# Kernel optimization log

Measured on AMD Instinct MI355X. Metric: run time of the kernel, lower is better.

The kernel has to match this reference:

```python
import jax, jax.numpy as jnp
import numpy as np

N = 10000      # nodes (drugs)
F_IN = 128     # input feature dim
H1 = 64        # hidden1
H2 = 32        # hidden2
R = 65         # num_relations
E_O = 320000   # edges in main graph
E_S = 160000   # edges per augmented subgraph
NB = 4         # num_layers parallel branches
B = 4096       # drug pairs


def setup_inputs() -> dict:
    key = jax.random.key(0)
    ks = jax.random.split(key, 32)
    def nrm(k, shape, fan_in):
        return (jax.random.normal(k, shape) * (1.0 / np.sqrt(fan_in))).astype(jnp.float32)
    inp = {}
    inp["x_o"] = jax.random.normal(ks[0], (N, F_IN), jnp.float32)
    inp["edge_index_o"] = jax.random.randint(ks[1], (2, E_O), 0, N)
    inp["edge_type_o"] = jax.random.randint(ks[2], (E_O,), 0, R)
    inp["x_s"] = jax.random.normal(ks[3], (NB, N, F_IN), jnp.float32)
    inp["edge_index_s"] = jax.random.randint(ks[4], (NB, 2, E_S), 0, N)
    inp["edge_type_s"] = jax.random.randint(ks[5], (NB, E_S), 0, R)
    inp["idx"] = jax.random.randint(ks[6], (2, B), 0, N)
    inp["features1"] = jax.random.normal(ks[7], (N, F_IN), jnp.float32)
    # main encoder RGCN params
    inp["W1"] = nrm(ks[8], (R, F_IN, H1), F_IN)
    inp["root1"] = nrm(ks[9], (F_IN, H1), F_IN)
    inp["b1"] = jnp.zeros((H1,), jnp.float32)
    inp["W2"] = nrm(ks[10], (R, H1, H2), H1)
    inp["root2"] = nrm(ks[11], (H1, H2), H1)
    inp["b2"] = jnp.zeros((H2,), jnp.float32)
    # 4 branch encoders (stacked over branch dim)
    inp["Ws1"] = nrm(ks[12], (NB, R, F_IN, H1), F_IN)
    inp["roots1"] = nrm(ks[13], (NB, F_IN, H1), F_IN)
    inp["bs1"] = jnp.zeros((NB, H1), jnp.float32)
    inp["Ws2"] = nrm(ks[14], (NB, R, H1, H2), H1)
    inp["roots2"] = nrm(ks[15], (NB, H1, H2), H1)
    inp["bs2"] = jnp.zeros((NB, H2), jnp.float32)
    # MLP head: 576 -> 256 -> 128 -> 65
    inp["mlp_w1"] = nrm(ks[16], (576, 256), 576)
    inp["mlp_b1"] = jnp.zeros((256,), jnp.float32)
    inp["mlp_w2"] = nrm(ks[17], (256, 128), 256)
    inp["mlp_b2"] = jnp.zeros((128,), jnp.float32)
    inp["mlp_w3"] = nrm(ks[18], (128, 65), 128)
    inp["mlp_b3"] = jnp.zeros((65,), jnp.float32)
    return inp


def _rgcn(x, src, dst, etype, W, Wroot, b):
    """PyG RGCNConv with aggr='mean': per-(dst,relation) mean of W_r x_j, summed over relations, plus root transform."""
    n = x.shape[0]
    r = W.shape[0]
    h = jnp.einsum('ni,rio->nro', x, W)                      # [N,R,out]
    seg = dst * r + etype                                    # per-(node,rel) segment id
    ones = jnp.ones(src.shape[0], x.dtype)
    deg = jax.ops.segment_sum(ones, seg, num_segments=n * r)  # in-degree per (dst,rel)
    norm = 1.0 / jnp.maximum(deg, 1.0)
    m = h[src, etype] * norm[seg][:, None]                   # [E,out]
    agg = jax.ops.segment_sum(m, dst, num_segments=n)        # scatter-add to dst
    return agg + x @ Wroot + b


def _branch(xb, src, dst, et, W1b, r1b, b1b, W2b, r2b, b2b):
    h1 = jax.nn.relu(_rgcn(xb, src, dst, et, W1b, r1b, b1b))
    return _rgcn(h1, src, dst, et, W2b, r2b, b2b)


def reference(x_o, edge_index_o, edge_type_o, x_s, edge_index_s, edge_type_s, idx,
              features1, W1, root1, b1, W2, root2, b2,
              Ws1, roots1, bs1, Ws2, roots2, bs2,
              mlp_w1, mlp_b1, mlp_w2, mlp_b2, mlp_w3, mlp_b3):
    # main encoder (dropout is eval-mode identity)
    src_o, dst_o = edge_index_o[0], edge_index_o[1]
    h1 = jax.nn.relu(_rgcn(x_o, src_o, dst_o, edge_type_o, W1, root1, b1))
    x2_oo = _rgcn(h1, src_o, dst_o, edge_type_o, W2, root2, b2)   # [N,H2]
    # 4 parallel branch encoders, vmapped over branch dim
    x2_s = jax.vmap(_branch)(x_s, edge_index_s[:, 0], edge_index_s[:, 1], edge_type_s,
                             Ws1, roots1, bs1, Ws2, roots2, bs2)  # [NB,N,H2]
    n = x2_oo.shape[0]
    embeds = jnp.concatenate(
        [x2_oo, jnp.transpose(x2_s, (1, 0, 2)).reshape(n, -1)], axis=1)  # [N, 5*H2]
    d1, d2 = idx[0], idx[1]
    feats = jnp.concatenate(
        [embeds[d1], features1[d1], embeds[d2], features1[d2]], axis=1)  # [B,576]
    h = jax.nn.elu(feats @ mlp_w1 + mlp_b1)
    h = jax.nn.elu(h @ mlp_w2 + mlp_b2)
    return h @ mlp_w3 + mlp_b3  # [B,65] logits
```

## Files before the change

kernel.cpp:

```cpp
#include <hip/hip_runtime.h>
#include <hip/hip_bf16.h>

namespace {
constexpr int N_NODES = 10000;
constexpr int FIN  = 128;
constexpr int H1S  = 64;
constexpr int H2S  = 32;
constexpr int RREL = 65;
constexpr int EO   = 320000;
constexpr int ES   = 160000;
constexpr int NBR  = 4;
constexpr int BP   = 4096;
constexpr int E_TOT = EO + 4 * ES;
constexpr int CAP_MAIN = EO + 128 * RREL;
constexpr int CAP_SUB  = ES + 128 * RREL;
constexpr int CAP_TOT  = CAP_MAIN + 4 * CAP_SUB;
constexpr int CHK_MAIN = CAP_MAIN / 128;
constexpr int CHK_SUB  = CAP_SUB / 128;
constexpr int CHK_TOT  = CHK_MAIN + 4 * CHK_SUB;
constexpr int CHK_TOT_PAD = 7840;
constexpr int SCH = 1024;
constexpr int SBLK_MAIN = (EO + SCH - 1) / SCH;
}

typedef unsigned short u16;
typedef unsigned int   u32;
typedef unsigned long long u64;
typedef short bf16x8 __attribute__((ext_vector_type(8)));
typedef float f32x4  __attribute__((ext_vector_type(4)));

__device__ __forceinline__ u16 f2bf(float f) {
    u32 u = __builtin_bit_cast(u32, f);
    u32 r = u + 0x7FFFu + ((u >> 16) & 1u);
    return (u16)(r >> 16);
}
__device__ __forceinline__ float bf2f_lo(u32 v) { return __builtin_bit_cast(float, v << 16); }
__device__ __forceinline__ float bf2f_hi(u32 v) { return __builtin_bit_cast(float, v & 0xFFFF0000u); }
__device__ __forceinline__ bf16x8 as_bf16x8(uint4 v) {
    union { uint4 u; bf16x8 b; } cv; cv.u = v; return cv.b;
}
__device__ __forceinline__ int chunk_graph(int bid) {
    return (bid < CHK_MAIN) ? 0 : 1 + (bid - CHK_MAIN) / CHK_SUB;
}

__global__ __launch_bounds__(256) void count_hist_all(const int* __restrict__ et_o,
                                                      const int* __restrict__ et_s,
                                                      int* __restrict__ hist) {
    int g = blockIdx.y;
    const int* etv; int E;
    if (g == 0) { etv = et_o; E = EO; }
    else { etv = et_s + (size_t)(g - 1) * ES; E = ES; }
    __shared__ int lh[RREL];
    for (int i = threadIdx.x; i < RREL; i += 256) lh[i] = 0;
    __syncthreads();
    for (int e = blockIdx.x * 256 + threadIdx.x; e < E; e += gridDim.x * 256)
        atomicAdd(&lh[etv[e]], 1);
    __syncthreads();
    for (int i = threadIdx.x; i < RREL; i += 256) {
        int c = lh[i];
        if (c) atomicAdd(&hist[g * RREL + i], c);
    }
}

__global__ void prefix_fill(const int* __restrict__ hist, int* __restrict__ cursor,
                            int* __restrict__ relbase, int* __restrict__ c2r) {
    int g = blockIdx.x;
    __shared__ int offs[RREL + 1];
    int capc  = (g == 0) ? CHK_MAIN : CHK_SUB;
    int cbase = (g == 0) ? 0 : CHK_MAIN + (g - 1) * CHK_SUB;
    int ebase = (g == 0) ? 0 : CAP_MAIN + (g - 1) * CAP_SUB;
    if (threadIdx.x == 0) {
        int acc = 0;
        for (int r = 0; r < RREL; ++r) {
            offs[r] = acc;
            cursor[g * RREL + r]  = ebase + acc;
            relbase[g * RREL + r] = ebase + acc;
            int c = hist[g * RREL + r];
            acc += (c + 127) & ~127;
        }
        offs[RREL] = acc;
    }
    __syncthreads();
    int total = offs[RREL];
    for (int c = threadIdx.x; c < capc; c += blockDim.x) {
        int pos = c * 128;
        int r = -1;
        if (pos < total) {
            int lo = 0, hi = RREL - 1;
            while (lo < hi) { int mid = (lo + hi + 1) >> 1; if (offs[mid] <= pos) lo = mid; else hi = mid - 1; }
            r = lo;
        }
        c2r[cbase + c] = r;
    }
}

__global__ __launch_bounds__(256) void scatter_rel(const int* __restrict__ ei_o,
                                                   const int* __restrict__ et_o,
                                                   const int* __restrict__ ei_s,
                                                   const int* __restrict__ et_s,
                                                   int* __restrict__ cursor,
                                                   int* __restrict__ ssrc,
                                                   int* __restrict__ sdst) {
    int g = blockIdx.y;
    const int* srcv; const int* dstv; const int* etv; int E;
    if (g == 0) { srcv = ei_o; dstv = ei_o + EO; etv = et_o; E = EO; }
    else {
        int b = g - 1;
        srcv = ei_s + (size_t)b * 2 * ES;
        dstv = srcv + ES;
        etv  = et_s + (size_t)b * ES;
        E = ES;
    }
    __shared__ int lh[RREL];
    __shared__ int lbase[RREL];
    int tid = threadIdx.x;
    int e0 = blockIdx.x * SCH;
    if (e0 >= E) return;
    int e1 = min(e0 + SCH, E);
    for (int i = tid; i < RREL; i += 256) lh[i] = 0;
    __syncthreads();
    for (int e = e0 + tid; e < e1; e += 256)
        atomicAdd(&lh[etv[e]], 1);
    __syncthreads();
    for (int i = tid; i < RREL; i += 256) {
        int c = lh[i];
        lbase[i] = c ? atomicAdd(&cursor[g * RREL + i], c) : 0;
        lh[i] = 0;
    }
    __syncthreads();
    for (int e = e0 + tid; e < e1; e += 256) {
        int r = etv[e];
        int rank = atomicAdd(&lh[r], 1);
        int pos = lbase[r] + rank;
        ssrc[pos] = srcv[e];
        sdst[pos] = dstv[e];
    }
}

__global__ __launch_bounds__(256) void seg_hist(const int* __restrict__ sdst,
                                                const int* __restrict__ relbase,
                                                const int* __restrict__ hist,
                                                u32* __restrict__ deg_r) {
    int r = blockIdx.x, g = blockIdx.y;
    __shared__ u32 h[N_NODES];
    int tid = threadIdx.x;
    for (int i = tid; i < N_NODES; i += 256) h[i] = 0;
    __syncthreads();
    int start = relbase[g * RREL + r], cnt = hist[g * RREL + r];
    for (int i = start + tid; i < start + cnt; i += 256)
        atomicAdd(&h[sdst[i]], 1u);
    __syncthreads();
    u32* out = deg_r + (size_t)(g * RREL + r) * N_NODES;
    for (int i = tid; i < N_NODES; i += 256) out[i] = h[i];
}

__global__ __launch_bounds__(256) void nodedeg_from_degr(const u32* __restrict__ deg_r,
                                                         int* __restrict__ node_deg) {
    int t = blockIdx.x * 256 + threadIdx.x;
    if (t >= 5 * N_NODES) return;
    int g = t / N_NODES, d = t % N_NODES;
    const u32* base = deg_r + (size_t)g * RREL * N_NODES + d;
    u32 s = 0;
    for (int r = 0; r < RREL; ++r) s += base[(size_t)r * N_NODES];
    node_deg[t] = (int)s;
}

__global__ __launch_bounds__(256) void scan_rowptr(const int* __restrict__ node_deg,
                                                   int* __restrict__ row_ptr) {
    int g = blockIdx.x;
    const int* nd = node_deg + (size_t)g * N_NODES;
    int* rp = row_ptr + (size_t)g * (N_NODES + 1);
    int off = (g == 0) ? 0 : EO + (g - 1) * ES;
    __shared__ int part[257];
    int tid = threadIdx.x;
    const int CH = (N_NODES + 255) / 256;
    int base = tid * CH;
    int s = 0;
    for (int i = 0; i < CH; ++i) { int ix = base + i; if (ix < N_NODES) s += nd[ix]; }
    part[tid + 1] = s;
    if (tid == 0) part[0] = 0;
    __syncthreads();
    if (tid == 0) { for (int i = 1; i <= 256; ++i) part[i] += part[i - 1]; }
    __syncthreads();
    int acc = part[tid];
    for (int i = 0; i < CH; ++i) {
        int ix = base + i;
        if (ix < N_NODES) { rp[ix] = off + acc; acc += nd[ix]; }
    }
    if (tid == 0) rp[N_NODES] = off + part[256];
}

__global__ __launch_bounds__(256) void drbase(const u32* __restrict__ deg_r,
                                              const int* __restrict__ row_ptr,
                                              u32* __restrict__ base_abs) {
    int t = blockIdx.x * 256 + threadIdx.x;
    if (t >= 5 * N_NODES) return;
    int g = t / N_NODES, d = t % N_NODES;
    u32 run = (u32)row_ptr[(size_t)g * (N_NODES + 1) + d];
    const u32* din = deg_r + (size_t)g * RREL * N_NODES + d;
    u32* bout = base_abs + (size_t)g * RREL * N_NODES + d;
    for (int r = 0; r < RREL; ++r) {
        bout[(size_t)r * N_NODES] = run;
        run += din[(size_t)r * N_NODES];
    }
}

__global__ __launch_bounds__(256) void snrm_epos(const int* __restrict__ sdst,
                                                 const int* __restrict__ relbase,
                                                 const int* __restrict__ hist,
                                                 const u32* __restrict__ base_abs,
                                                 const u32* __restrict__ deg_r,
                                                 int* __restrict__ epos,
                                                 float* __restrict__ snrm) {
    int r = blockIdx.x, g = blockIdx.y;
    int cnt = hist[g * RREL + r];
    if (cnt == 0) return;
    __shared__ u32 cur[N_NODES];
    __shared__ u16 dg[N_NODES];
    int tid = threadIdx.x;
    const u32* bslice = base_abs + (size_t)(g * RREL + r) * N_NODES;
    const u32* dslice = deg_r + (size_t)(g * RREL + r) * N_NODES;
    for (int i = tid; i < N_NODES; i += 256) {
        cur[i] = bslice[i];
        dg[i] = (u16)dslice[i];
    }
    __syncthreads();
    int start = relbase[g * RREL + r];
    for (int pos = start + tid; pos < start + cnt; pos += 256) {
        int d = sdst[pos];
        u32 slot = atomicAdd(&cur[d], 1u);
        epos[pos] = (int)slot;
        snrm[pos] = 1.0f / fmaxf((float)dg[d], 1.0f);
    }
}

namespace {
constexpr int NX_  = 5 * N_NODES * FIN;
constexpr int NW1_ = 5 * RREL * FIN * H1S;
constexpr int NW2_ = 5 * RREL * H1S * H2S;
constexpr int NM1_ = 256 * 576;
constexpr int NM2_ = 128 * 256;
constexpr int NM3_ = 128 * 128;
constexpr int NPREP = NX_ + NW1_ + NW2_ + NM1_ + NM2_ + NM3_;
}
__global__ __launch_bounds__(256) void prep_all(const float* __restrict__ x_o,
                                                const float* __restrict__ x_s,
                                                const float* __restrict__ W1,
                                                const float* __restrict__ Ws1,
                                                const float* __restrict__ W2,
                                                const float* __restrict__ Ws2,
                                                const float* __restrict__ mw1,
                                                const float* __restrict__ mw2,
                                                const float* __restrict__ mw3,
                                                u16* __restrict__ xbf,
                                                u16* __restrict__ wt1,
                                                u16* __restrict__ wt2,
                                                u16* __restrict__ w1t,
                                                u16* __restrict__ w2t,
                                                u16* __restrict__ w3t) {
    int t = blockIdx.x * 256 + threadIdx.x;
    if (t < NX_) {
        int g = t / (N_NODES * FIN), off = t % (N_NODES * FIN);
        float v = (g == 0) ? x_o[off] : x_s[(size_t)(g - 1) * N_NODES * FIN + off];
        xbf[t] = f2bf(v);
        return;
    }
    t -= NX_;
    if (t < NW1_) {
        int q = t % (RREL * FIN * H1S), g = t / (RREL * FIN * H1S);
        int k = q & 127; int ro = q >> 7; int o = ro & 63; int r = ro >> 6;
        const float* src = (g == 0) ? W1 : Ws1 + (size_t)(g - 1) * RREL * FIN * H1S;
        wt1[(size_t)g * RREL * FIN * H1S + q] = f2bf(src[((size_t)r * FIN + k) * H1S + o]);
        return;
    }
    t -= NW1_;
    if (t < NW2_) {
        int q = t % (RREL * H1S * H2S), g = t / (RREL * H1S * H2S);
        int k = q & 63; int ro = q >> 6; int o = ro & 31; int r = ro >> 5;
        const float* src = (g == 0) ? W2 : Ws2 + (size_t)(g - 1) * RREL * H1S * H2S;
        wt2[(size_t)g * RREL * H1S * H2S + q] = f2bf(src[((size_t)r * H1S + k) * H2S + o]);
        return;
    }
    t -= NW2_;
    if (t < NM1_) {
        int k = t % 576, o = t / 576;
        w1t[t] = f2bf(mw1[(size_t)k * 256 + o]);
        return;
    }
    t -= NM1_;
    if (t < NM2_) {
        int k = t % 256, o = t / 256;
        w2t[t] = f2bf(mw2[(size_t)k * 128 + o]);
        return;
    }
    t -= NM2_;
    if (t < NM3_) {
        int k = t % 128, o = t / 128;
        w3t[t] = (o < 65) ? f2bf(mw3[(size_t)k * 65 + o]) : (u16)0;
    }
}

__global__ __launch_bounds__(256) void rgcn_mfma_l1_all(const u16* __restrict__ xbfa,
                                                        const int* __restrict__ ssrc,
                                                        const float* __restrict__ snrm,
                                                        const int* __restrict__ c2r,
                                                        const int* __restrict__ epos,
                                                        const u16* __restrict__ wt1a,
                                                        u16* __restrict__ medge) {
    __shared__ uint4 Wt4[64 * 16];
    int tid = threadIdx.x;
    int bid = blockIdx.x;
    int r = c2r[bid];
    if (r < 0) return;
    int g = chunk_graph(bid);
    int e0 = bid * 128;
    const u16* xbf = xbfa + (size_t)g * N_NODES * FIN;
    {
        const uint4* wsrc = (const uint4*)(wt1a + ((size_t)g * RREL + r) * H1S * FIN);
        #pragma unroll
        for (int i = 0; i < 4; ++i) {
            int g16 = tid + i * 256;
            int row = g16 >> 4, c = g16 & 15;
            Wt4[row * 16 + (c ^ (row & 7))] = wsrc[g16];
        }
    }
    int w = tid >> 6, l = tid & 63;
    int lo = l & 15, hi = l >> 4;
    int ea = w * 32 + lo, eb = ea + 16;
    int sa = ssrc[e0 + ea], sb = ssrc[e0 + eb];
    const uint4* xa = (const uint4*)(xbf + (size_t)sa * FIN);
    const uint4* xb = (const uint4*)(xbf + (size_t)sb * FIN);
    __syncthreads();
    f32x4 acc[2][4];
    #pragma unroll
    for (int m = 0; m < 2; ++m)
        #pragma unroll
        for (int n = 0; n < 4; ++n) acc[m][n] = {0.f, 0.f, 0.f, 0.f};
    #pragma unroll
    for (int kk = 0; kk < 4; ++kk) {
        int kc = kk * 4 + hi;
        bf16x8 a0 = as_bf16x8(xa[kc]);
        bf16x8 a1 = as_bf16x8(xb[kc]);
        #pragma unroll
        for (int n = 0; n < 4; ++n) {
            int o = n * 16 + lo;
            bf16x8 b = as_bf16x8(Wt4[o * 16 + (kc ^ (o & 7))]);
            acc[0][n] = __builtin_amdgcn_mfma_f32_16x16x32_bf16(a0, b, acc[0][n], 0, 0, 0);
            acc[1][n] = __builtin_amdgcn_mfma_f32_16x16x32_bf16(a1, b, acc[1][n], 0, 0, 0);
        }
    }
    #pragma unroll
    for (int m = 0; m < 2; ++m) {
        #pragma unroll
        for (int rg = 0; rg < 4; ++rg) {
            int erow = e0 + w * 32 + m * 16 + hi * 4 + rg;
            float nv = snrm[erow];
            if (nv != 0.f) {
                size_t jb = (size_t)epos[erow] * H1S;
                #pragma unroll
                for (int n = 0; n < 4; ++n)
                    __builtin_nontemporal_store(f2bf(acc[m][n][rg] * nv),
                                                medge + jb + n * 16 + lo);
            }
        }
    }
}

__global__ __launch_bounds__(256) void rgcn_mfma_l2_all(const u16* __restrict__ h1bfa,
                                                        const int* __restrict__ ssrc,
                                                        const float* __restrict__ snrm,
                                                        const int* __restrict__ c2r,
                                                        const int* __restrict__ epos,
                                                        const u16* __restrict__ wt2a,
                                                        u16* __restrict__ medge) {
    __shared__ uint4 Wt4[32 * 8];
    int tid = threadIdx.x;
    int bid = blockIdx.x;
    int r = c2r[bid];
    if (r < 0) return;
    int g = chunk_graph(bid);
    int e0 = bid * 128;
    const u16* h1bf = h1bfa + (size_t)g * N_NODES * H1S;
    {
        const uint4* wsrc = (const uint4*)(wt2a + ((size_t)g * RREL + r) * H2S * H1S);
        int row = tid >> 3, c = tid & 7;
        Wt4[row * 8 + (c ^ (row & 7))] = wsrc[tid];
    }
    int w = tid >> 6, l = tid & 63;
    int lo = l & 15, hi = l >> 4;
    int ea = w * 32 + lo, eb = ea + 16;
    int sa = ssrc[e0 + ea], sb = ssrc[e0 + eb];
    const uint4* xa = (const uint4*)(h1bf + (size_t)sa * H1S);
    const uint4* xb = (const uint4*)(h1bf + (size_t)sb * H1S);
    __syncthreads();
    f32x4 acc[2][2];
    #pragma unroll
    for (int m = 0; m < 2; ++m)
        #pragma unroll
        for (int n = 0; n < 2; ++n) acc[m][n] = {0.f, 0.f, 0.f, 0.f};
    #pragma unroll
    for (int kk = 0; kk < 2; ++kk) {
        int kc = kk * 4 + hi;
        bf16x8 a0 = as_bf16x8(xa[kc]);
        bf16x8 a1 = as_bf16x8(xb[kc]);
        #pragma unroll
        for (int n = 0; n < 2; ++n) {
            int o = n * 16 + lo;
            bf16x8 b = as_bf16x8(Wt4[o * 8 + (kc ^ (o & 7))]);
            acc[0][n] = __builtin_amdgcn_mfma_f32_16x16x32_bf16(a0, b, acc[0][n], 0, 0, 0);
            acc[1][n] = __builtin_amdgcn_mfma_f32_16x16x32_bf16(a1, b, acc[1][n], 0, 0, 0);
        }
    }
    #pragma unroll
    for (int m = 0; m < 2; ++m) {
        #pragma unroll
        for (int rg = 0; rg < 4; ++rg) {
            int erow = e0 + w * 32 + m * 16 + hi * 4 + rg;
            float nv = snrm[erow];
            if (nv != 0.f) {
                size_t jb = (size_t)epos[erow] * H2S;
                #pragma unroll
                for (int n = 0; n < 2; ++n)
                    __builtin_nontemporal_store(f2bf(acc[m][n][rg] * nv),
                                                medge + jb + n * 16 + lo);
            }
        }
    }
}

__global__ __launch_bounds__(256) void finish_l1_all(const float* __restrict__ x_o,
                                                     const float* __restrict__ x_s,
                                                     const float* __restrict__ root1,
                                                     const float* __restrict__ roots1,
                                                     const float* __restrict__ b1,
                                                     const float* __restrict__ bs1,
                                                     const u16* __restrict__ medge,
                                                     const int* __restrict__ row_ptr,
                                                     float* __restrict__ aggH1,
                                                     u16* __restrict__ h1bfa) {
    int g = blockIdx.y;
    const float* x    = (g == 0) ? x_o : x_s + (size_t)(g - 1) * N_NODES * FIN;
    const float* root = (g == 0) ? root1 : roots1 + (size_t)(g - 1) * FIN * H1S;
    const float* bias = (g == 0) ? b1 : bs1 + (size_t)(g - 1) * H1S;
    const int* rp = row_ptr + (size_t)g * (N_NODES + 1);
    float* h1 = aggH1 + (size_t)g * N_NODES * H1S;
    u16* h1bf = h1bfa + (size_t)g * N_NODES * H1S;
    __shared__ float xs[16][FIN + 1];
    int tid = threadIdx.x;
    int vsub = tid >> 4, og = tid & 15;
    int v = blockIdx.x * 16 + vsub;
    bool valid = v < N_NODES;
    int vv = valid ? v : N_NODES - 1;
    #pragma unroll
    for (int i = 0; i < 8; ++i)
        xs[vsub][og + 16 * i] = x[(size_t)vv * FIN + og + 16 * i];
    int j0 = rp[vv], j1 = rp[vv + 1];
    float4 acc;
    acc.x = bias[og * 4 + 0]; acc.y = bias[og * 4 + 1];
    acc.z = bias[og * 4 + 2]; acc.w = bias[og * 4 + 3];
    for (int j = j0; j < j1; ++j) {
        u64 m = __builtin_nontemporal_load(
            (const u64*)(medge + (size_t)j * H1S + og * 4));
        u32 mlo = (u32)m, mhi = (u32)(m >> 32);
        acc.x += bf2f_lo(mlo); acc.y += bf2f_hi(mlo);
        acc.z += bf2f_lo(mhi); acc.w += bf2f_hi(mhi);
    }
    __syncthreads();
    const float* Rp = root + og * 4;
    #pragma unroll 16
    for (int i = 0; i < FIN; ++i) {
        float xv = xs[vsub][i];
        float4 w = *(const float4*)(Rp + (size_t)i * H1S);
        acc.x += xv * w.x; acc.y += xv * w.y; acc.z += xv * w.z; acc.w += xv * w.w;
    }
    if (valid) {
        float r0 = fmaxf(acc.x, 0.f), r1 = fmaxf(acc.y, 0.f);
        float r2 = fmaxf(acc.z, 0.f), r3 = fmaxf(acc.w, 0.f);
        float* ag = h1 + (size_t)vv * H1S + og * 4;
        ag[0] = r0; ag[1] = r1; ag[2] = r2; ag[3] = r3;
        uint2 pk;
        pk.x = (u32)f2bf(r0) | ((u32)f2bf(r1) << 16);
        pk.y = (u32)f2bf(r2) | ((u32)f2bf(r3) << 16);
        *(uint2*)(h1bf + (size_t)vv * H1S + og * 4) = pk;
    }
}

__global__ __launch_bounds__(256) void finish_l2_all(const float* __restrict__ aggH1,
                                                     const float* __restrict__ root2,
                                                     const float* __restrict__ roots2,
                                                     const float* __restrict__ b2,
                                                     const float* __restrict__ bs2,
                                                     const u16* __restrict__ medge,
                                                     const int* __restrict__ row_ptr,
                                                     float* __restrict__ aggH2) {
    int g = blockIdx.y;
    const float* x    = aggH1 + (size_t)g * N_NODES * H1S;
    const float* root = (g == 0) ? root2 : roots2 + (size_t)(g - 1) * H1S * H2S;
    const float* bias = (g == 0) ? b2 : bs2 + (size_t)(g - 1) * H2S;
    const int* rp = row_ptr + (size_t)g * (N_NODES + 1);
    float* x2 = aggH2 + (size_t)g * N_NODES * H2S;
    __shared__ float xs[32][H1S + 1];
    int tid = threadIdx.x;
    int vsub = tid >> 3, og = tid & 7;
    int v = blockIdx.x * 32 + vsub;
    bool valid = v < N_NODES;
    int vv = valid ? v : N_NODES - 1;
    #pragma unroll
    for (int i = 0; i < 8; ++i)
        xs[vsub][og + 8 * i] = x[(size_t)vv * H1S + og + 8 * i];
    int j0 = rp[vv], j1 = rp[vv + 1];
    float4 acc;
    acc.x = bias[og * 4 + 0]; acc.y = bias[og * 4 + 1];
    acc.z = bias[og * 4 + 2]; acc.w = bias[og * 4 + 3];
    for (int j = j0; j < j1; ++j) {
        u64 m = __builtin_nontemporal_load(
            (const u64*)(medge + (size_t)j * H2S + og * 4));
        u32 mlo = (u32)m, mhi = (u32)(m >> 32);
        acc.x += bf2f_lo(mlo); acc.y += bf2f_hi(mlo);
        acc.z += bf2f_lo(mhi); acc.w += bf2f_hi(mhi);
    }
    __syncthreads();
    const float* Rp = root + og * 4;
    #pragma unroll
    for (int i = 0; i < H1S; ++i) {
        float xv = xs[vsub][i];
        float4 w = *(const float4*)(Rp + (size_t)i * H2S);
        acc.x += xv * w.x; acc.y += xv * w.y; acc.z += xv * w.z; acc.w += xv * w.w;
    }
    if (valid) {
        float* ag = x2 + (size_t)vv * H2S + og * 4;
        ag[0] = acc.x; ag[1] = acc.y; ag[2] = acc.z; ag[3] = acc.w;
    }
}

__global__ __launch_bounds__(256) void gather_feats_direct(const float* __restrict__ aggH2,
                                                           const float* __restrict__ features1,
                                                           const int* __restrict__ idx,
                                                           u16* __restrict__ featsbf) {
    int t = blockIdx.x * blockDim.x + threadIdx.x;
    if (t >= BP * 576) return;
    int b = t / 576, c = t % 576;
    int d1 = idx[b], d2 = idx[BP + b];
    float v;
    if (c < 160) {
        int bb = c >> 5, cc = c & 31;
        v = aggH2[(size_t)bb * N_NODES * H2S + (size_t)d1 * H2S + cc];
    } else if (c < 288) {
        v = features1[(size_t)d1 * FIN + (c - 160)];
    } else if (c < 448) {
        int cc2 = c - 288;
        int bb = cc2 >> 5, cc = cc2 & 31;
        v = aggH2[(size_t)bb * N_NODES * H2S + (size_t)d2 * H2S + cc];
    } else {
        v = features1[(size_t)d2 * FIN + (c - 448)];
    }
    featsbf[t] = f2bf(v);
}

template <int ACT, int OUTF>
__global__ __launch_bounds__(256) void mlp_mfma(const u16* __restrict__ A,
                                                const u16* __restrict__ Bt,
                                                const float* __restrict__ bias,
                                                u16* __restrict__ Cbf,
                                                float* __restrict__ Cf,
                                                int M, int N, int K) {
    __shared__ uint4 As4[128 * 8];
    __shared__ uint4 Bs4[64 * 8];
    int tid = threadIdx.x;
    int row0 = blockIdx.x * 128, col0 = blockIdx.y * 64;
    int w = tid >> 6, l = tid & 63;
    int lo = l & 15, hi = l >> 4;
    f32x4 acc[2][4];
    #pragma unroll
    for (int m = 0; m < 2; ++m)
        #pragma unroll
        for (int n = 0; n < 4; ++n) acc[m][n] = {0.f, 0.f, 0.f, 0.f};
    int nchunks = K >> 6;
    for (int ch = 0; ch < nchunks; ++ch) {
        #pragma unroll
        for (int i = 0; i < 4; ++i) {
            int g16 = tid + i * 256;
            int rr = g16 >> 3, c = g16 & 7;
            As4[rr * 8 + (c ^ (rr & 7))] =
                *((const uint4*)(A + (size_t)(row0 + rr) * K + ch * 64) + c);
        }
        #pragma unroll
        for (int i = 0; i < 2; ++i) {
            int g16 = tid + i * 256;
            int rr = g16 >> 3, c = g16 & 7;
            Bs4[rr * 8 + (c ^ (rr & 7))] =
                *((const uint4*)(Bt + (size_t)(col0 + rr) * K + ch * 64) + c);
        }
        __syncthreads();
        #pragma unroll
        for (int ks = 0; ks < 2; ++ks) {
            int kc = ks * 4 + hi;
            int ra = w * 32 + lo, rb = w * 32 + 16 + lo;
            bf16x8 a0 = as_bf16x8(As4[ra * 8 + (kc ^ (ra & 7))]);
            bf16x8 a1 = as_bf16x8(As4[rb * 8 + (kc ^ (rb & 7))]);
            #pragma unroll
            for (int n = 0; n < 4; ++n) {
                int o = n * 16 + lo;
                bf16x8 b = as_bf16x8(Bs4[o * 8 + (kc ^ (o & 7))]);
                acc[0][n] = __builtin_amdgcn_mfma_f32_16x16x32_bf16(a0, b, acc[0][n], 0, 0, 0);
                acc[1][n] = __builtin_amdgcn_mfma_f32_16x16x32_bf16(a1, b, acc[1][n], 0, 0, 0);
            }
        }
        __syncthreads();
    }
    #pragma unroll
    for (int m = 0; m < 2; ++m) {
        #pragma unroll
        for (int rg = 0; rg < 4; ++rg) {
            int rr = row0 + w * 32 + m * 16 + hi * 4 + rg;
            if (rr < M) {
                #pragma unroll
                for (int n = 0; n < 4; ++n) {
                    int cc = col0 + n * 16 + lo;
                    if (cc < N) {
                        float v = acc[m][n][rg] + bias[cc];
                        if (ACT == 1) v = (v > 0.f) ? v : expm1f(v);
                        if (OUTF) Cf[(size_t)rr * N + cc] = v;
                        else Cbf[(size_t)rr * N + cc] = f2bf(v);
                    }
                }
            }
        }
    }
}

extern "C" void kernel_launch(void* const* d_in, const int* in_sizes, int n_in,
                              void* d_out, int out_size, void* d_ws, size_t ws_size,
                              hipStream_t stream) {
    const float* x_o      = (const float*)d_in[0];
    const int*   ei_o     = (const int*)d_in[1];
    const int*   et_o     = (const int*)d_in[2];
    const float* x_s      = (const float*)d_in[3];
    const int*   ei_s     = (const int*)d_in[4];
    const int*   et_s     = (const int*)d_in[5];
    const int*   idx      = (const int*)d_in[6];
    const float* features1= (const float*)d_in[7];
    const float* W1       = (const float*)d_in[8];
    const float* root1    = (const float*)d_in[9];
    const float* b1       = (const float*)d_in[10];
    const float* W2       = (const float*)d_in[11];
    const float* root2    = (const float*)d_in[12];
    const float* b2       = (const float*)d_in[13];
    const float* Ws1      = (const float*)d_in[14];
    const float* roots1   = (const float*)d_in[15];
    const float* bs1      = (const float*)d_in[16];
    const float* Ws2      = (const float*)d_in[17];
    const float* roots2   = (const float*)d_in[18];
    const float* bs2      = (const float*)d_in[19];
    const float* mlp_w1   = (const float*)d_in[20];
    const float* mlp_b1   = (const float*)d_in[21];
    const float* mlp_w2   = (const float*)d_in[22];
    const float* mlp_b2   = (const float*)d_in[23];
    const float* mlp_w3   = (const float*)d_in[24];
    const float* mlp_b3   = (const float*)d_in[25];

    int*   hist     = (int*)d_ws;
    int*   ssrc     = hist + 5 * RREL;
    float* snrm     = (float*)(ssrc + CAP_TOT);
    int*   sdst     = (int*)(snrm + CAP_TOT);
    int*   cursor   = sdst + CAP_TOT;
    int*   relbase  = cursor + 5 * RREL;
    int*   c2r      = relbase + 5 * RREL;
    u32*   deg_r    = (u32*)(c2r + CHK_TOT_PAD);
    u32*   base_abs = deg_r + (size_t)5 * RREL * N_NODES;
    int*   node_deg = (int*)(base_abs + (size_t)5 * RREL * N_NODES);
    int*   row_ptr  = node_deg + 5 * N_NODES;
    int*   epos     = row_ptr + 5 * (N_NODES + 1);
    float* aggH1    = (float*)(epos + CAP_TOT);
    float* aggH2    = aggH1 + (size_t)5 * N_NODES * H1S;
    u16*   featsbf  = (u16*)(aggH2 + (size_t)5 * N_NODES * H2S);
    u16*   mh1bf    = featsbf + (size_t)BP * 576;
    u16*   mh2bf    = mh1bf + (size_t)BP * 256;
    u16*   w1t      = mh2bf + (size_t)BP * 128;
    u16*   w2t      = w1t + (size_t)256 * 576;
    u16*   w3t      = w2t + (size_t)128 * 256;
    u16*   wt1a     = w3t + (size_t)128 * 128;
    u16*   wt2a     = wt1a + (size_t)5 * RREL * H1S * FIN;
    u16*   xbfa     = wt2a + (size_t)5 * RREL * H2S * H1S;
    u16*   h1bfa    = xbfa + (size_t)5 * N_NODES * FIN;
    u16*   medge    = h1bfa + (size_t)5 * N_NODES * H1S;

    size_t zero_bytes = (size_t)((char*)sdst - (char*)d_ws);
    hipMemsetAsync(d_ws, 0, zero_bytes, stream);

    prep_all<<<(NPREP + 255) / 256, 256, 0, stream>>>(
        x_o, x_s, W1, Ws1, W2, Ws2, mlp_w1, mlp_w2, mlp_w3,
        xbfa, wt1a, wt2a, w1t, w2t, w3t);
    count_hist_all<<<dim3(128, 5), 256, 0, stream>>>(et_o, et_s, hist);
    prefix_fill<<<5, 256, 0, stream>>>(hist, cursor, relbase, c2r);
    scatter_rel<<<dim3(SBLK_MAIN, 5), 256, 0, stream>>>(
        ei_o, et_o, ei_s, et_s, cursor, ssrc, sdst);
    seg_hist<<<dim3(RREL, 5), 256, 0, stream>>>(sdst, relbase, hist, deg_r);
    nodedeg_from_degr<<<(5 * N_NODES + 255) / 256, 256, 0, stream>>>(deg_r, node_deg);
    scan_rowptr<<<5, 256, 0, stream>>>(node_deg, row_ptr);
    drbase<<<(5 * N_NODES + 255) / 256, 256, 0, stream>>>(deg_r, row_ptr, base_abs);
    snrm_epos<<<dim3(RREL, 5), 256, 0, stream>>>(
        sdst, relbase, hist, base_abs, deg_r, epos, snrm);

    rgcn_mfma_l1_all<<<CHK_TOT, 256, 0, stream>>>(
        xbfa, ssrc, snrm, c2r, epos, wt1a, medge);
    finish_l1_all<<<dim3((N_NODES + 15) / 16, 5), 256, 0, stream>>>(
        x_o, x_s, root1, roots1, b1, bs1, medge, row_ptr, aggH1, h1bfa);
    rgcn_mfma_l2_all<<<CHK_TOT, 256, 0, stream>>>(
        h1bfa, ssrc, snrm, c2r, epos, wt2a, medge);
    finish_l2_all<<<dim3((N_NODES + 31) / 32, 5), 256, 0, stream>>>(
        aggH1, root2, roots2, b2, bs2, medge, row_ptr, aggH2);

    gather_feats_direct<<<(BP * 576 + 255) / 256, 256, 0, stream>>>(aggH2, features1, idx, featsbf);
    mlp_mfma<1, 0><<<dim3(BP / 128, 4), 256, 0, stream>>>(featsbf, w1t, mlp_b1, mh1bf, nullptr, BP, 256, 576);
    mlp_mfma<1, 0><<<dim3(BP / 128, 2), 256, 0, stream>>>(mh1bf, w2t, mlp_b2, mh2bf, nullptr, BP, 128, 256);
    mlp_mfma<0, 1><<<dim3(BP / 128, 2), 256, 0, stream>>>(mh2bf, w3t, mlp_b3, nullptr, (float*)d_out, BP, 65, 128);
}
```

Measured before the change: 488.4 us.

## Stage gathered source rows in LDS and swizzle chunk blocks across XCDs

The layer-1 and layer-2 edge MFMA kernels now gather source-node feature rows cooperatively into swizzled shared memory. Two threads fetch each row with contiguous 64-byte reads, replacing the per-lane scattered 16-byte global loads that fed the MFMA fragments. Layer 1 stages its 128-wide rows in two halves to limit shared memory, which adds extra barriers. Block IDs are also remapped so that consecutive chunks, which share a relation weight and graph, land on the same XCD to improve L2 reuse of weights and features.

After: 519.0 us. +6.3%, slower.

```diff
diff --git a/kernel.cpp b/kernel.cpp
--- a/kernel.cpp
+++ b/kernel.cpp
@@ -41,6 +41,11 @@
 }
 __device__ __forceinline__ int chunk_graph(int bid) {
     return (bid < CHK_MAIN) ? 0 : 1 + (bid - CHK_MAIN) / CHK_SUB;
+}
+__device__ __forceinline__ int xcd_swz(int bid) {
+    constexpr int q = CHK_TOT / 8, rr = CHK_TOT % 8;
+    int x = bid & 7, i = bid >> 3;
+    return (x < rr ? x * (q + 1) : rr * (q + 1) + (x - rr) * q) + i;
 }
 
 __global__ __launch_bounds__(256) void count_hist_all(const int* __restrict__ et_o,
@@ -308,8 +313,9 @@
                                                         const u16* __restrict__ wt1a,
                                                         u16* __restrict__ medge) {
     __shared__ uint4 Wt4[64 * 16];
-    int tid = threadIdx.x;
-    int bid = blockIdx.x;
+    __shared__ uint4 Xs4[128 * 8];
+    int tid = threadIdx.x;
+    int bid = xcd_swz(blockIdx.x);
     int r = c2r[bid];
     if (r < 0) return;
     int g = chunk_graph(bid);
@@ -326,27 +332,37 @@
     }
     int w = tid >> 6, l = tid & 63;
     int lo = l & 15, hi = l >> 4;
-    int ea = w * 32 + lo, eb = ea + 16;
-    int sa = ssrc[e0 + ea], sb = ssrc[e0 + eb];
-    const uint4* xa = (const uint4*)(xbf + (size_t)sa * FIN);
-    const uint4* xb = (const uint4*)(xbf + (size_t)sb * FIN);
-    __syncthreads();
+    int rt = tid >> 1, ph = tid & 1;
+    int srow = ssrc[e0 + rt];
+    const uint4* xsrc = (const uint4*)(xbf + (size_t)srow * FIN);
     f32x4 acc[2][4];
     #pragma unroll
     for (int m = 0; m < 2; ++m)
         #pragma unroll
         for (int n = 0; n < 4; ++n) acc[m][n] = {0.f, 0.f, 0.f, 0.f};
     #pragma unroll
-    for (int kk = 0; kk < 4; ++kk) {
-        int kc = kk * 4 + hi;
-        bf16x8 a0 = as_bf16x8(xa[kc]);
-        bf16x8 a1 = as_bf16x8(xb[kc]);
-        #pragma unroll
-        for (int n = 0; n < 4; ++n) {
-            int o = n * 16 + lo;
-            bf16x8 b = as_bf16x8(Wt4[o * 16 + (kc ^ (o & 7))]);
-            acc[0][n] = __builtin_amdgcn_mfma_f32_16x16x32_bf16(a0, b, acc[0][n], 0, 0, 0);
-            acc[1][n] = __builtin_amdgcn_mfma_f32_16x16x32_bf16(a1, b, acc[1][n], 0, 0, 0);
+    for (int khalf = 0; khalf < 2; ++khalf) {
+        if (khalf) __syncthreads();
+        #pragma unroll
+        for (int j = 0; j < 4; ++j) {
+            int c = ph * 4 + j;
+            Xs4[rt * 8 + (c ^ (rt & 7))] = xsrc[khalf * 8 + c];
+        }
+        __syncthreads();
+        #pragma unroll
+        for (int kk2 = 0; kk2 < 2; ++kk2) {
+            int kc  = kk2 * 4 + hi;
+            int kcg = khalf * 8 + kc;
+            int ea = w * 32 + lo, eb = ea + 16;
+            bf16x8 a0 = as_bf16x8(Xs4[ea * 8 + (kc ^ (ea & 7))]);
+            bf16x8 a1 = as_bf16x8(Xs4[eb * 8 + (kc ^ (eb & 7))]);
+            #pragma unroll
+            for (int n = 0; n < 4; ++n) {
+                int o = n * 16 + lo;
+                bf16x8 b = as_bf16x8(Wt4[o * 16 + (kcg ^ (o & 7))]);
+                acc[0][n] = __builtin_amdgcn_mfma_f32_16x16x32_bf16(a0, b, acc[0][n], 0, 0, 0);
+                acc[1][n] = __builtin_amdgcn_mfma_f32_16x16x32_bf16(a1, b, acc[1][n], 0, 0, 0);
+            }
         }
     }
     #pragma unroll
@@ -373,9 +389,10 @@
                                                         const int* __restrict__ epos,
                                                         const u16* __restrict__ wt2a,
                                                         u16* __restrict__ medge) {
+    __shared__ uint4 Xs4[128 * 8];
     __shared__ uint4 Wt4[32 * 8];
     int tid = threadIdx.x;
-    int bid = blockIdx.x;
+    int bid = xcd_swz(blockIdx.x);
     int r = c2r[bid];
     if (r < 0) return;
     int g = chunk_graph(bid);
@@ -386,13 +403,19 @@
         int row = tid >> 3, c = tid & 7;
         Wt4[row * 8 + (c ^ (row & 7))] = wsrc[tid];
     }
+    {
+        int rt = tid >> 1, h = tid & 1;
+        int s = ssrc[e0 + rt];
+        const uint4* src = (const uint4*)(h1bf + (size_t)s * H1S) + h * 4;
+        #pragma unroll
+        for (int j = 0; j < 4; ++j) {
+            int c = h * 4 + j;
+            Xs4[rt * 8 + (c ^ (rt & 7))] = src[j];
+        }
+    }
+    __syncthreads();
     int w = tid >> 6, l = tid & 63;
     int lo = l & 15, hi = l >> 4;
-    int ea = w * 32 + lo, eb = ea + 16;
-    int sa = ssrc[e0 + ea], sb = ssrc[e0 + eb];
-    const uint4* xa = (const uint4*)(h1bf + (size_t)sa * H1S);
-    const uint4* xb = (const uint4*)(h1bf + (size_t)sb * H1S);
-    __syncthreads();
     f32x4 acc[2][2];
     #pragma unroll
     for (int m = 0; m < 2; ++m)
@@ -401,8 +424,9 @@
     #pragma unroll
     for (int kk = 0; kk < 2; ++kk) {
         int kc = kk * 4 + hi;
-        bf16x8 a0 = as_bf16x8(xa[kc]);
-        bf16x8 a1 = as_bf16x8(xb[kc]);
+        int ea = w * 32 + lo, eb = ea + 16;
+        bf16x8 a0 = as_bf16x8(Xs4[ea * 8 + (kc ^ (ea & 7))]);
+        bf16x8 a1 = as_bf16x8(Xs4[eb * 8 + (kc ^ (eb & 7))]);
         #pragma unroll
         for (int n = 0; n < 2; ++n) {
             int o = n * 16 + lo;
```
